# Optimization experiments

Hardware: AMD Instinct MI355X
Metric: run time of the kernel (lower is better)

The kernel has to match this reference:

```python
import jax, jax.numpy as jnp
import numpy as np

D_MODEL = 1024
NHEAD = 16
D_K = D_MODEL // NHEAD


def setup_inputs() -> dict:
    key = jax.random.key(0)
    ks = jax.random.split(key, 12)
    B, S = 1, 4096
    s = 1.0 / np.sqrt(D_MODEL)
    inp = {
        "query": jax.random.normal(ks[0], (B, S, D_MODEL), jnp.float32),
        "key": jax.random.normal(ks[1], (B, S, D_MODEL), jnp.float32),
        "value": jax.random.normal(ks[2], (B, S, D_MODEL), jnp.float32),
        "W_q": jax.random.normal(ks[3], (D_MODEL, D_MODEL), jnp.float32) * s,
        "b_q": jnp.zeros((D_MODEL,), jnp.float32),
        "W_k": jax.random.normal(ks[4], (D_MODEL, D_MODEL), jnp.float32) * s,
        "b_k": jnp.zeros((D_MODEL,), jnp.float32),
        "W_v": jax.random.normal(ks[5], (D_MODEL, D_MODEL), jnp.float32) * s,
        "b_v": jnp.zeros((D_MODEL,), jnp.float32),
        "W_o": jax.random.normal(ks[6], (D_MODEL, D_MODEL), jnp.float32) * s,
        "b_o": jnp.zeros((D_MODEL,), jnp.float32),
    }
    return inp


def reference(query, key, value, W_q, b_q, W_k, b_k, W_v, b_v, W_o, b_o):
    B, S, _ = query.shape
    # linear projections (torch Linear: x @ W.T + b)
    Q = query @ W_q.T + b_q
    K = key @ W_k.T + b_k
    V = value @ W_v.T + b_v
    # split heads: [B, S, D] -> [B, H, S, d_k]
    Q = Q.reshape(B, S, NHEAD, D_K).transpose(0, 2, 1, 3)
    K = K.reshape(B, S, NHEAD, D_K).transpose(0, 2, 1, 3)
    V = V.reshape(B, S, NHEAD, D_K).transpose(0, 2, 1, 3)
    # scaled dot-product attention (materializes [B,H,S,S] like original)
    scores = jnp.einsum("bhqd,bhkd->bhqk", Q, K) / jnp.sqrt(jnp.float32(D_K))
    weights = jax.nn.softmax(scores, axis=-1)
    attn = jnp.einsum("bhqk,bhkd->bhqd", weights, V)
    # combine heads: [B, H, S, d_k] -> [B, S, D]
    attn = attn.transpose(0, 2, 1, 3).reshape(B, S, D_MODEL)
    return attn @ W_o.T + b_o
```

## Files before the change

kernel.cpp:

```cpp
#include <hip/hip_runtime.h>
#include <hip/hip_bf16.h>
#include <type_traits>

constexpr int SEQ = 4096;
constexpr int DMODEL = 1024;
constexpr int NH = 16;
constexpr int DKH = 64;
constexpr float SCALE = 0.125f;
constexpr float SCALE2 = 0.125f * 1.4426950408889634f;

typedef __bf16 bf16x8 __attribute__((ext_vector_type(8)));
typedef __bf16 bf16x4 __attribute__((ext_vector_type(4)));
typedef float f32x4 __attribute__((ext_vector_type(4)));
typedef float f32x16 __attribute__((ext_vector_type(16)));
typedef unsigned int u32x4 __attribute__((ext_vector_type(4)));
union W8 { u32x4 u; bf16x8 v; };

__device__ inline void store_c(__hip_bfloat16* p, float v) { *p = __float2bfloat16(v); }
__device__ inline void store_c(float* p, float v) { *p = v; }

typedef const void __attribute__((address_space(1)))* gas_ptr;
typedef void __attribute__((address_space(3)))* las_ptr;
__device__ inline void load_lds_16B(const void* g, void* l) {
  __builtin_amdgcn_global_load_lds((gas_ptr)g, (las_ptr)l, 16, 0, 0);
}

__device__ inline unsigned pack2(float a, float b) {
  union { __bf16 h[2]; unsigned u; } p;
  p.h[0] = (__bf16)a; p.h[1] = (__bf16)b;
  return p.u;
}

__device__ inline void st8(__hip_bfloat16* buf, int row, int col, bf16x8 v) {
  *(bf16x8*)(buf + row * 64 + (col ^ ((row & 7) << 3))) = v;
}
__device__ inline bf16x8 ld8(const __hip_bfloat16* buf, int row, int col) {
  return *(const bf16x8*)(buf + row * 64 + (col ^ ((row & 7) << 3)));
}

__global__ __launch_bounds__(256)
void cvt_all(const float* __restrict__ q, const float* __restrict__ k,
             const float* __restrict__ v, const float* __restrict__ wq,
             const float* __restrict__ wk, const float* __restrict__ wv,
             const float* __restrict__ wo,
             __bf16* __restrict__ Xq, __bf16* __restrict__ Xk,
             __bf16* __restrict__ Xv, __bf16* __restrict__ Wqb,
             __bf16* __restrict__ Wkb, __bf16* __restrict__ Wvb,
             __bf16* __restrict__ Wob) {
  const int b = blockIdx.x;
  const float* src; __bf16* dst; size_t base;
  if      (b < 2048) { src = q;  dst = Xq;  base = b; }
  else if (b < 4096) { src = k;  dst = Xk;  base = b - 2048; }
  else if (b < 6144) { src = v;  dst = Xv;  base = b - 4096; }
  else if (b < 6656) { src = wq; dst = Wqb; base = b - 6144; }
  else if (b < 7168) { src = wk; dst = Wkb; base = b - 6656; }
  else if (b < 7680) { src = wv; dst = Wvb; base = b - 7168; }
  else               { src = wo; dst = Wob; base = b - 7680; }
  const size_t i = (base * 256 + threadIdx.x) * 8;
  const float4 a = *(const float4*)(src + i);
  const float4 c = *(const float4*)(src + i + 4);
  bf16x8 r = {(__bf16)a.x, (__bf16)a.y, (__bf16)a.z, (__bf16)a.w,
              (__bf16)c.x, (__bf16)c.y, (__bf16)c.z, (__bf16)c.w};
  *(bf16x8*)(dst + i) = r;
}

constexpr int BK = 64;

template <typename TC, bool TRANS_C>
__global__ __launch_bounds__(256)
void gemm128(const __bf16* __restrict__ A,
             const __bf16* __restrict__ W,
             const float* __restrict__ bias,
             TC* __restrict__ C,
             float out_scale) {
  __shared__ alignas(16) __bf16 As[128][64];
  __shared__ alignas(16) __bf16 Ws[64][64];

  const int t = threadIdx.x;
  const int lane = t & 63;
  const int w = t >> 6;
  const int wr = w >> 1;
  const int wc = w & 1;
  const int col = lane & 15;
  const int quad = lane >> 4;
  const int m_blk = blockIdx.y * 128;
  const int n_blk = blockIdx.x * 64;

  const int srow = t >> 3;
  const int scol = (t & 7) * 8;

  f32x4 acc[4][2] = {};

  for (int k0 = 0; k0 < DMODEL; k0 += BK) {
    __syncthreads();
    #pragma unroll
    for (int p = 0; p < 4; ++p)
      load_lds_16B(A + (size_t)(m_blk + p * 32 + srow) * DMODEL + k0 + scol,
                   &As[p * 32 + srow][scol]);
    #pragma unroll
    for (int p = 0; p < 2; ++p)
      load_lds_16B(W + (size_t)(n_blk + p * 32 + srow) * DMODEL + k0 + scol,
                   &Ws[p * 32 + srow][scol]);
    __syncthreads();

    #pragma unroll
    for (int kh = 0; kh < BK; kh += 32) {
      bf16x8 af[4], bfr[2];
      #pragma unroll
      for (int at = 0; at < 4; ++at)
        af[at] = *(const bf16x8*)&As[wr * 64 + at * 16 + col][kh + quad * 8];
      #pragma unroll
      for (int bt = 0; bt < 2; ++bt)
        bfr[bt] = *(const bf16x8*)&Ws[wc * 32 + bt * 16 + col][kh + quad * 8];
      #pragma unroll
      for (int at = 0; at < 4; ++at)
        #pragma unroll
        for (int bt = 0; bt < 2; ++bt)
          acc[at][bt] = __builtin_amdgcn_mfma_f32_16x16x32_bf16(
              af[at], bfr[bt], acc[at][bt], 0, 0, 0);
    }
  }

  #pragma unroll
  for (int at = 0; at < 4; ++at) {
    #pragma unroll
    for (int bt = 0; bt < 2; ++bt) {
      const int n = n_blk + wc * 32 + bt * 16 + col;
      const float b = bias[n];
      #pragma unroll
      for (int i = 0; i < 4; ++i) {
        const int m = m_blk + wr * 64 + at * 16 + quad * 4 + i;
        const float v = (acc[at][bt][i] + b) * out_scale;
        if constexpr (TRANS_C) store_c(&C[(size_t)n * SEQ + m], v);
        else                   store_c(&C[(size_t)m * DMODEL + n], v);
      }
    }
  }
}

__global__ __launch_bounds__(256)
void gemm_qkv(const __bf16* __restrict__ Xq, const __bf16* __restrict__ Xk,
              const __bf16* __restrict__ Xv, const __bf16* __restrict__ Wq,
              const __bf16* __restrict__ Wk, const __bf16* __restrict__ Wv,
              const float* __restrict__ bq, const float* __restrict__ bk,
              const float* __restrict__ bv,
              __hip_bfloat16* __restrict__ Cq, __hip_bfloat16* __restrict__ Ck,
              __hip_bfloat16* __restrict__ Cv) {
  __shared__ alignas(16) __bf16 As[128][64];
  __shared__ alignas(16) __bf16 Ws[64][64];

  const int z = blockIdx.z;
  const __bf16* A = (z == 0) ? Xq : (z == 1) ? Xk : Xv;
  const __bf16* W = (z == 0) ? Wq : (z == 1) ? Wk : Wv;
  const float* bias = (z == 0) ? bq : (z == 1) ? bk : bv;
  __hip_bfloat16* C = (z == 0) ? Cq : (z == 1) ? Ck : Cv;
  const float out_scale = (z == 0) ? SCALE2 : 1.0f;

  const int t = threadIdx.x;
  const int lane = t & 63;
  const int w = t >> 6;
  const int wr = w >> 1;
  const int wc = w & 1;
  const int col = lane & 15;
  const int quad = lane >> 4;
  const int m_blk = blockIdx.y * 128;
  const int n_blk = blockIdx.x * 64;

  const int srow = t >> 3;
  const int scol = (t & 7) * 8;

  f32x4 acc[4][2] = {};

  for (int k0 = 0; k0 < DMODEL; k0 += BK) {
    __syncthreads();
    #pragma unroll
    for (int p = 0; p < 4; ++p)
      load_lds_16B(A + (size_t)(m_blk + p * 32 + srow) * DMODEL + k0 + scol,
                   &As[p * 32 + srow][scol]);
    #pragma unroll
    for (int p = 0; p < 2; ++p)
      load_lds_16B(W + (size_t)(n_blk + p * 32 + srow) * DMODEL + k0 + scol,
                   &Ws[p * 32 + srow][scol]);
    __syncthreads();

    #pragma unroll
    for (int kh = 0; kh < BK; kh += 32) {
      bf16x8 af[4], bfr[2];
      #pragma unroll
      for (int at = 0; at < 4; ++at)
        af[at] = *(const bf16x8*)&As[wr * 64 + at * 16 + col][kh + quad * 8];
      #pragma unroll
      for (int bt = 0; bt < 2; ++bt)
        bfr[bt] = *(const bf16x8*)&Ws[wc * 32 + bt * 16 + col][kh + quad * 8];
      #pragma unroll
      for (int at = 0; at < 4; ++at)
        #pragma unroll
        for (int bt = 0; bt < 2; ++bt)
          acc[at][bt] = __builtin_amdgcn_mfma_f32_16x16x32_bf16(
              af[at], bfr[bt], acc[at][bt], 0, 0, 0);
    }
  }

  #pragma unroll
  for (int at = 0; at < 4; ++at) {
    #pragma unroll
    for (int bt = 0; bt < 2; ++bt) {
      const int n = n_blk + wc * 32 + bt * 16 + col;
      const float b = bias[n];
      #pragma unroll
      for (int i = 0; i < 4; ++i) {
        const int m = m_blk + wr * 64 + at * 16 + quad * 4 + i;
        const float v = (acc[at][bt][i] + b) * out_scale;
        if (z == 2) C[(size_t)n * SEQ + m] = __float2bfloat16(v);
        else        C[(size_t)m * DMODEL + n] = __float2bfloat16(v);
      }
    }
  }
}

constexpr int LDK = 72;

template <typename TA, typename TC, bool TRANS_C>
__global__ __launch_bounds__(256)
void gemm_tiled(const TA* __restrict__ A,
                const float* __restrict__ W,
                const float* __restrict__ bias,
                TC* __restrict__ C,
                float out_scale) {
  __shared__ alignas(16) __bf16 As[128][LDK];
  __shared__ alignas(16) __bf16 Ws[64][LDK];

  const int t = threadIdx.x;
  const int lane = t & 63;
  const int w = t >> 6;
  const int wr = w >> 1;
  const int wc = w & 1;
  const int col = lane & 15;
  const int quad = lane >> 4;
  const int m_blk = blockIdx.y * 128;
  const int n_blk = blockIdx.x * 64;

  f32x4 acc[4][2] = {};

  for (int k0 = 0; k0 < DMODEL; k0 += BK) {
    __syncthreads();
    if constexpr (std::is_same<TA, float>::value) {
      #pragma unroll
      for (int p = 0; p < 8; ++p) {
        const int r = p * 16 + (t >> 4);
        const int c = (t & 15) * 4;
        const float4 v =
            *(const float4*)(A + (size_t)(m_blk + r) * DMODEL + k0 + c);
        bf16x4 b = {(__bf16)v.x, (__bf16)v.y, (__bf16)v.z, (__bf16)v.w};
        *(bf16x4*)&As[r][c] = b;
      }
    } else {
      #pragma unroll
      for (int p = 0; p < 4; ++p) {
        const int r = p * 32 + (t >> 3);
        const int c = (t & 7) * 8;
        *(bf16x8*)&As[r][c] =
            *(const bf16x8*)((const __bf16*)A + (size_t)(m_blk + r) * DMODEL + k0 + c);
      }
    }
    #pragma unroll
    for (int p = 0; p < 4; ++p) {
      const int r = p * 16 + (t >> 4);
      const int c = (t & 15) * 4;
      const float4 v =
          *(const float4*)(W + (size_t)(n_blk + r) * DMODEL + k0 + c);
      bf16x4 b = {(__bf16)v.x, (__bf16)v.y, (__bf16)v.z, (__bf16)v.w};
      *(bf16x4*)&Ws[r][c] = b;
    }
    __syncthreads();

    #pragma unroll
    for (int kh = 0; kh < BK; kh += 32) {
      bf16x8 af[4], bfr[2];
      #pragma unroll
      for (int at = 0; at < 4; ++at)
        af[at] = *(const bf16x8*)&As[wr * 64 + at * 16 + col][kh + quad * 8];
      #pragma unroll
      for (int bt = 0; bt < 2; ++bt)
        bfr[bt] = *(const bf16x8*)&Ws[wc * 32 + bt * 16 + col][kh + quad * 8];
      #pragma unroll
      for (int at = 0; at < 4; ++at)
        #pragma unroll
        for (int bt = 0; bt < 2; ++bt)
          acc[at][bt] = __builtin_amdgcn_mfma_f32_16x16x32_bf16(
              af[at], bfr[bt], acc[at][bt], 0, 0, 0);
    }
  }

  #pragma unroll
  for (int at = 0; at < 4; ++at) {
    #pragma unroll
    for (int bt = 0; bt < 2; ++bt) {
      const int n = n_blk + wc * 32 + bt * 16 + col;
      const float b = bias[n];
      #pragma unroll
      for (int i = 0; i < 4; ++i) {
        const int m = m_blk + wr * 64 + at * 16 + quad * 4 + i;
        const float v = (acc[at][bt][i] + b) * out_scale;
        if constexpr (TRANS_C) store_c(&C[(size_t)n * SEQ + m], v);
        else                   store_c(&C[(size_t)m * DMODEL + n], v);
      }
    }
  }
}

__global__ __launch_bounds__(256, 4)
void flash_attn_splitN(const __hip_bfloat16* __restrict__ Q,
                       const __hip_bfloat16* __restrict__ K,
                       const __hip_bfloat16* __restrict__ Vt,
                       __hip_bfloat16* __restrict__ Op0,
                       __hip_bfloat16* __restrict__ Op1,
                       __hip_bfloat16* __restrict__ Op2,
                       __hip_bfloat16* __restrict__ Op3,
                       float* __restrict__ lsum_g) {
  __shared__ alignas(16) __hip_bfloat16 kt[64 * 64];
  __shared__ alignas(16) __hip_bfloat16 vtt[64 * 64];

  const int t = threadIdx.x;
  const int lane = t & 63;
  const int w = t >> 6;
  const int head = blockIdx.y;
  const int q0 = blockIdx.x * 128;
  const int z = blockIdx.z;
  const int nz = gridDim.z;
  const int l31 = lane & 31;
  const int hl = lane >> 5;

  __hip_bfloat16* O = (z == 0) ? Op0 : (z == 1) ? Op1 : (z == 2) ? Op2 : Op3;

  bf16x8 qf[4];
  {
    const __hip_bfloat16* qp =
        Q + (size_t)(q0 + w * 32 + l31) * DMODEL + head * DKH + hl * 8;
    #pragma unroll
    for (int db = 0; db < 4; ++db) qf[db] = *(const bf16x8*)(qp + db * 16);
  }

  f32x16 acc_o[2] = {};
  float lsa = 0.f, lsb = 0.f;

  const int sr = t >> 2;
  const int sc = (t & 3) * 16;
  const int seg = SEQ / nz;
  const int NT = seg / 64;
  const int kbeg = z * seg;

  const __hip_bfloat16* kgp = K + (size_t)(kbeg + sr) * DMODEL + head * DKH + sc;
  const __hip_bfloat16* vgp = Vt + (size_t)(head * DKH + sr) * SEQ + kbeg + sc;

  bf16x8 kr0 = *(const bf16x8*)kgp;
  bf16x8 kr1 = *(const bf16x8*)(kgp + 8);
  bf16x8 vr0 = *(const bf16x8*)vgp;
  bf16x8 vr1 = *(const bf16x8*)(vgp + 8);

  for (int ti = 0; ti < NT; ++ti) {
    __syncthreads();
    st8(kt, sr, sc, kr0);  st8(kt, sr, sc + 8, kr1);
    st8(vtt, sr, sc, vr0); st8(vtt, sr, sc + 8, vr1);
    __syncthreads();

    if (ti + 1 < NT) {
      const __hip_bfloat16* kn = kgp + (size_t)(ti + 1) * 64 * DMODEL;
      const __hip_bfloat16* vn = vgp + (ti + 1) * 64;
      kr0 = *(const bf16x8*)kn; kr1 = *(const bf16x8*)(kn + 8);
      vr0 = *(const bf16x8*)vn; vr1 = *(const bf16x8*)(vn + 8);
    }

    bf16x8 pa[4];
    #pragma unroll
    for (int kb = 0; kb < 2; ++kb) {
      f32x16 s = {};
      __builtin_amdgcn_s_setprio(1);
      #pragma unroll
      for (int db = 0; db < 4; ++db) {
        const bf16x8 kf = ld8(kt, kb * 32 + l31, db * 16 + hl * 8);
        s = __builtin_amdgcn_mfma_f32_32x32x16_bf16(kf, qf[db], s, 0, 0, 0);
      }
      __builtin_amdgcn_s_setprio(0);
      unsigned wp[8];
      #pragma unroll
      for (int i = 0; i < 8; ++i) {
        const float p0 = __builtin_amdgcn_exp2f(s[2 * i]);
        const float p1 = __builtin_amdgcn_exp2f(s[2 * i + 1]);
        lsa += p0; lsb += p1;
        wp[i] = pack2(p0, p1);
      }
      #pragma unroll
      for (int b = 0; b < 2; ++b) {
        unsigned a0 = wp[4 * b + 0], a2 = wp[4 * b + 2];
        unsigned a1 = wp[4 * b + 1], a3 = wp[4 * b + 3];
        asm("v_permlane32_swap_b32 %0, %1" : "+v"(a0), "+v"(a2));
        asm("v_permlane32_swap_b32 %0, %1" : "+v"(a1), "+v"(a3));
        W8 u;
        u.u[0] = a0; u.u[1] = a1; u.u[2] = a2; u.u[3] = a3;
        pa[kb * 2 + b] = u.v;
      }
    }

    __builtin_amdgcn_s_setprio(1);
    #pragma unroll
    for (int kq = 0; kq < 4; ++kq)
      #pragma unroll
      for (int db = 0; db < 2; ++db) {
        const bf16x8 vb = ld8(vtt, db * 32 + l31, kq * 16 + hl * 8);
        acc_o[db] = __builtin_amdgcn_mfma_f32_32x32x16_bf16(
            pa[kq], vb, acc_o[db], 0, 0, 0);
      }
    __builtin_amdgcn_s_setprio(0);
  }

  float lsumq = lsa + lsb;
  lsumq += __shfl_xor(lsumq, 32);
  if (lane < 32)
    lsum_g[((size_t)z * NH + head) * SEQ + q0 + w * 32 + lane] = lsumq;

  #pragma unroll
  for (int db = 0; db < 2; ++db) {
    #pragma unroll
    for (int r = 0; r < 16; ++r) {
      const int qr = q0 + w * 32 + (r & 3) + 8 * (r >> 2) + 4 * hl;
      const int c = head * DKH + db * 32 + l31;
      O[(size_t)qr * DMODEL + c] = __float2bfloat16(acc_o[db][r]);
    }
  }
}

__global__ __launch_bounds__(256)
void attn_combine(const __hip_bfloat16* __restrict__ Op0,
                  const __hip_bfloat16* __restrict__ Op1,
                  const __hip_bfloat16* __restrict__ Op2,
                  const __hip_bfloat16* __restrict__ Op3,
                  const float* __restrict__ ls,
                  __hip_bfloat16* __restrict__ Ao, int nz) {
  const size_t i = ((size_t)blockIdx.x * 256 + threadIdx.x) * 8;
  const int qrow = (int)(i >> 10);
  const int h = (int)((i & 1023) >> 6);
  float lsum = ls[(size_t)h * SEQ + qrow] +
               ls[(size_t)(NH + h) * SEQ + qrow];
  const bf16x8 a = *(const bf16x8*)(Op0 + i);
  const bf16x8 b = *(const bf16x8*)(Op1 + i);
  float s[8];
  #pragma unroll
  for (int j = 0; j < 8; ++j) s[j] = (float)a[j] + (float)b[j];
  if (nz == 4) {
    lsum += ls[(size_t)(2 * NH + h) * SEQ + qrow] +
            ls[(size_t)(3 * NH + h) * SEQ + qrow];
    const bf16x8 c = *(const bf16x8*)(Op2 + i);
    const bf16x8 d = *(const bf16x8*)(Op3 + i);
    #pragma unroll
    for (int j = 0; j < 8; ++j) s[j] += (float)c[j] + (float)d[j];
  }
  const float inv = 1.f / lsum;
  bf16x8 r;
  #pragma unroll
  for (int j = 0; j < 8; ++j) r[j] = (__bf16)(s[j] * inv);
  *(bf16x8*)(Ao + i) = r;
}

constexpr int LDP = 72;
constexpr float SHIFT = 8.0f;

__global__ __launch_bounds__(256)
void flash_attn_mono(const __hip_bfloat16* __restrict__ Q,
                     const __hip_bfloat16* __restrict__ K,
                     const __hip_bfloat16* __restrict__ Vt,
                     __hip_bfloat16* __restrict__ O) {
  __shared__ alignas(16) __hip_bfloat16 kt[64][LDP];
  __shared__ alignas(16) __hip_bfloat16 vtt[DKH][LDP];
  __shared__ alignas(16) __hip_bfloat16 plT[4][32][LDP];

  const int t = threadIdx.x;
  const int lane = t & 63;
  const int w = t >> 6;
  const int h = blockIdx.y;
  const int q0 = blockIdx.x * 128;
  const int col = lane & 15;
  const int quad = lane >> 4;

  bf16x8 qf[2][2];
  #pragma unroll
  for (int rg = 0; rg < 2; ++rg) {
    const __hip_bfloat16* qptr =
        Q + (size_t)(q0 + w * 32 + rg * 16 + col) * DMODEL + h * DKH + quad * 8;
    qf[rg][0] = *(const bf16x8*)qptr;
    qf[rg][1] = *(const bf16x8*)(qptr + 32);
  }

  f32x4 acc_o[2][4] = {};
  float lsumq[2] = {0.f, 0.f};
  const int sr = t >> 2;
  const int sc = (t & 3) * 16;

  for (int k0 = 0; k0 < SEQ; k0 += 64) {
    __syncthreads();
    const __hip_bfloat16* kg = K + (size_t)(k0 + sr) * DMODEL + h * DKH + sc;
    *(bf16x8*)&kt[sr][sc]     = *(const bf16x8*)kg;
    *(bf16x8*)&kt[sr][sc + 8] = *(const bf16x8*)(kg + 8);
    const __hip_bfloat16* vg = Vt + (size_t)(h * DKH + sr) * SEQ + k0 + sc;
    *(bf16x8*)&vtt[sr][sc]     = *(const bf16x8*)vg;
    *(bf16x8*)&vtt[sr][sc + 8] = *(const bf16x8*)(vg + 8);
    __syncthreads();

    #pragma unroll
    for (int jt = 0; jt < 4; ++jt) {
      const bf16x8 kf0 = *(const bf16x8*)&kt[jt * 16 + col][quad * 8];
      const bf16x8 kf1 = *(const bf16x8*)&kt[jt * 16 + col][quad * 8 + 32];
      #pragma unroll
      for (int rg = 0; rg < 2; ++rg) {
        f32x4 zz = {0.f, 0.f, 0.f, 0.f};
        zz = __builtin_amdgcn_mfma_f32_16x16x32_bf16(kf0, qf[rg][0], zz, 0, 0, 0);
        zz = __builtin_amdgcn_mfma_f32_16x16x32_bf16(kf1, qf[rg][1], zz, 0, 0, 0);
        bf16x4 pk;
        #pragma unroll
        for (int r = 0; r < 4; ++r) {
          const float p = __expf(zz[r] - SHIFT);
          lsumq[rg] += p;
          pk[r] = (__bf16)p;
        }
        *(bf16x4*)&plT[w][rg * 16 + col][jt * 16 + quad * 4] = pk;
      }
    }

    bf16x8 pa[2][2];
    #pragma unroll
    for (int rg = 0; rg < 2; ++rg) {
      pa[rg][0] = *(const bf16x8*)&plT[w][rg * 16 + col][quad * 8];
      pa[rg][1] = *(const bf16x8*)&plT[w][rg * 16 + col][quad * 8 + 32];
    }
    #pragma unroll
    for (int jt = 0; jt < 4; ++jt) {
      const bf16x8 vb0 = *(const bf16x8*)&vtt[jt * 16 + col][quad * 8];
      const bf16x8 vb1 = *(const bf16x8*)&vtt[jt * 16 + col][quad * 8 + 32];
      #pragma unroll
      for (int rg = 0; rg < 2; ++rg) {
        acc_o[rg][jt] = __builtin_amdgcn_mfma_f32_16x16x32_bf16(
            pa[rg][0], vb0, acc_o[rg][jt], 0, 0, 0);
        acc_o[rg][jt] = __builtin_amdgcn_mfma_f32_16x16x32_bf16(
            pa[rg][1], vb1, acc_o[rg][jt], 0, 0, 0);
      }
    }
  }

  #pragma unroll
  for (int rg = 0; rg < 2; ++rg) {
    lsumq[rg] += __shfl_xor(lsumq[rg], 16);
    lsumq[rg] += __shfl_xor(lsumq[rg], 32);
  }
  float invr[2][4];
  #pragma unroll
  for (int rg = 0; rg < 2; ++rg)
    #pragma unroll
    for (int r = 0; r < 4; ++r)
      invr[rg][r] = 1.f / __shfl(lsumq[rg], quad * 4 + r);

  #pragma unroll
  for (int rg = 0; rg < 2; ++rg) {
    #pragma unroll
    for (int jt = 0; jt < 4; ++jt) {
      #pragma unroll
      for (int r = 0; r < 4; ++r) {
        const int qr = q0 + w * 32 + rg * 16 + quad * 4 + r;
        const int c = h * DKH + jt * 16 + col;
        O[(size_t)qr * DMODEL + c] = __float2bfloat16(acc_o[rg][jt][r] * invr[rg][r]);
      }
    }
  }
}

extern "C" void kernel_launch(void* const* d_in, const int* in_sizes, int n_in,
                              void* d_out, int out_size, void* d_ws, size_t ws_size,
                              hipStream_t stream) {
  const float* query = (const float*)d_in[0];
  const float* key   = (const float*)d_in[1];
  const float* value = (const float*)d_in[2];
  const float* W_q   = (const float*)d_in[3];
  const float* b_q   = (const float*)d_in[4];
  const float* W_k   = (const float*)d_in[5];
  const float* b_k   = (const float*)d_in[6];
  const float* W_v   = (const float*)d_in[7];
  const float* b_v   = (const float*)d_in[8];
  const float* W_o   = (const float*)d_in[9];
  const float* b_o   = (const float*)d_in[10];

  float* out = (float*)d_out;
  const size_t mat = (size_t)SEQ * DMODEL;
  const size_t MB = 1024 * 1024;

  char* ws = (char*)d_ws;
  __hip_bfloat16* Qp = (__hip_bfloat16*)d_out;
  __hip_bfloat16* Kp = (__hip_bfloat16*)ws;
  __hip_bfloat16* Vt = Kp + mat;

  dim3 gblock(256);

  if (ws_size >= 40 * MB) {
    __bf16* Xq  = (__bf16*)((char*)d_out + 8 * MB);
    __bf16* Xk  = (__bf16*)(ws + 16 * MB);
    __bf16* Xv  = (__bf16*)(ws + 24 * MB);
    __bf16* Wqb = (__bf16*)(ws + 32 * MB);
    __bf16* Wkb = (__bf16*)(ws + 34 * MB);
    __bf16* Wvb = (__bf16*)(ws + 36 * MB);
    __bf16* Wob = (__bf16*)(ws + 38 * MB);
    __hip_bfloat16* Op0 = (__hip_bfloat16*)(ws + 16 * MB);
    __hip_bfloat16* Op1 = (__hip_bfloat16*)(ws + 24 * MB);
    __hip_bfloat16* Op2 = (__hip_bfloat16*)((char*)d_out + 8 * MB);
    __hip_bfloat16* Op3 = (__hip_bfloat16*)(ws + 40 * MB);
    float* lsum = (float*)(ws + 33 * MB);
    __hip_bfloat16* Ao = (__hip_bfloat16*)(ws + 16 * MB);

    const int nz = (ws_size >= 48 * MB) ? 4 : 2;

    hipLaunchKernelGGL(cvt_all, dim3(8192), gblock, 0, stream,
                       query, key, value, W_q, W_k, W_v, W_o,
                       Xq, Xk, Xv, Wqb, Wkb, Wvb, Wob);

    dim3 qkvgrid(DMODEL / 64, SEQ / 128, 3);
    hipLaunchKernelGGL(gemm_qkv, qkvgrid, gblock, 0, stream,
                       Xq, Xk, Xv, Wqb, Wkb, Wvb, b_q, b_k, b_v,
                       Qp, Kp, Vt);

    dim3 agrid(SEQ / 128, NH, nz);
    hipLaunchKernelGGL(flash_attn_splitN, agrid, gblock, 0, stream,
                       Qp, Kp, Vt, Op0, Op1, Op2, Op3, lsum);
    hipLaunchKernelGGL(attn_combine, dim3(2048), gblock, 0, stream,
                       Op0, Op1, Op2, Op3, lsum, Ao, nz);

    dim3 ogrid(DMODEL / 64, SEQ / 128);
    hipLaunchKernelGGL((gemm128<float, false>), ogrid, gblock, 0, stream,
                       (const __bf16*)Ao, Wob, b_o, out, 1.0f);
  } else {
    __hip_bfloat16* Ao = Qp + mat;
    float* Cw = (float*)d_ws;
    dim3 fgrid(DMODEL / 64, SEQ / 128);
    hipLaunchKernelGGL((gemm_tiled<float, __hip_bfloat16, false>), fgrid, gblock,
                       0, stream, query, W_q, b_q, Qp, SCALE);
    hipLaunchKernelGGL((gemm_tiled<float, __hip_bfloat16, false>), fgrid, gblock,
                       0, stream, key, W_k, b_k, Kp, 1.0f);
    hipLaunchKernelGGL((gemm_tiled<float, __hip_bfloat16, true>), fgrid, gblock,
                       0, stream, value, W_v, b_v, Vt, 1.0f);
    dim3 agrid(SEQ / 128, NH);
    hipLaunchKernelGGL(flash_attn_mono, agrid, gblock, 0, stream, Qp, Kp, Vt, Ao);
    hipLaunchKernelGGL((gemm_tiled<__hip_bfloat16, float, false>), fgrid, gblock,
                       0, stream, Ao, W_o, b_o, Cw, 1.0f);
    hipMemcpyAsync(out, Cw, mat * sizeof(float), hipMemcpyDeviceToDevice, stream);
  }
}
```

Baseline: 278.1 us.

## Remap block indices per XCD for L2 locality and double-buffer attention K/V tiles

Block indices in the GEMM, QKV GEMM and flash attention kernels are remapped so that blocks landing on the same XCD (assumed round-robin L&7) share contiguous M rows or head/split pairs, to improve L2 reuse of A/K/V. The attention kernel also gains double-buffered LDS for K and V tiles, so the next tile is written to the spare buffer while the current one is consumed, and one barrier per iteration replaces two. This doubles the attention LDS footprint, which may reduce occupancy under launch_bounds(256,4), and the remap relies on specific grid shapes.

```diff
diff --git a/kernel.cpp b/kernel.cpp
--- a/kernel.cpp
+++ b/kernel.cpp
@@ -83,8 +83,12 @@
   const int wc = w & 1;
   const int col = lane & 15;
   const int quad = lane >> 4;
-  const int m_blk = blockIdx.y * 128;
-  const int n_blk = blockIdx.x * 64;
+
+  const int L = blockIdx.x + 16 * blockIdx.y;
+  const int xcd = L & 7;
+  const int c = L >> 3;
+  const int m_blk = (xcd * 4 + (c >> 4)) * 128;
+  const int n_blk = (c & 15) * 64;
 
   const int srow = t >> 3;
   const int scol = (t & 7) * 8;
@@ -149,12 +153,91 @@
   __shared__ alignas(16) __bf16 As[128][64];
   __shared__ alignas(16) __bf16 Ws[64][64];
 
-  const int z = blockIdx.z;
+  const int L = blockIdx.x + 16 * (blockIdx.y + 32 * blockIdx.z);
+  const int xcd = L & 7;
+  const int cc = L >> 3;
+  const int z = cc / 64;
+  const int c2 = cc & 63;
+  const int m_blk = (xcd * 4 + (c2 >> 4)) * 128;
+  const int n_blk = (c2 & 15) * 64;
+
   const __bf16* A = (z == 0) ? Xq : (z == 1) ? Xk : Xv;
   const __bf16* W = (z == 0) ? Wq : (z == 1) ? Wk : Wv;
   const float* bias = (z == 0) ? bq : (z == 1) ? bk : bv;
   __hip_bfloat16* C = (z == 0) ? Cq : (z == 1) ? Ck : Cv;
   const float out_scale = (z == 0) ? SCALE2 : 1.0f;
+
+  const int t = threadIdx.x;
+  const int lane = t & 63;
+  const int w = t >> 6;
+  const int wr = w >> 1;
+  const int wc = w & 1;
+  const int col = lane & 15;
+  const int quad = lane >> 4;
+
+  const int srow = t >> 3;
+  const int scol = (t & 7) * 8;
+
+  f32x4 acc[4][2] = {};
+
+  for (int k0 = 0; k0 < DMODEL; k0 += BK) {
+    __syncthreads();
+    #pragma unroll
+    for (int p = 0; p < 4; ++p)
+      load_lds_16B(A + (size_t)(m_blk + p * 32 + srow) * DMODEL + k0 + scol,
+                   &As[p * 32 + srow][scol]);
+    #pragma unroll
+    for (int p = 0; p < 2; ++p)
+      load_lds_16B(W + (size_t)(n_blk + p * 32 + srow) * DMODEL + k0 + scol,
+                   &Ws[p * 32 + srow][scol]);
+    __syncthreads();
+
+    #pragma unroll
+    for (int kh = 0; kh < BK; kh += 32) {
+      bf16x8 af[4], bfr[2];
+      #pragma unroll
+      for (int at = 0; at < 4; ++at)
+        af[at] = *(const bf16x8*)&As[wr * 64 + at * 16 + col][kh + quad * 8];
+      #pragma unroll
+      for (int bt = 0; bt < 2; ++bt)
+        bfr[bt] = *(const bf16x8*)&Ws[wc * 32 + bt * 16 + col][kh + quad * 8];
+      #pragma unroll
+      for (int at = 0; at < 4; ++at)
+        #pragma unroll
+        for (int bt = 0; bt < 2; ++bt)
+          acc[at][bt] = __builtin_amdgcn_mfma_f32_16x16x32_bf16(
+              af[at], bfr[bt], acc[at][bt], 0, 0, 0);
+    }
+  }
+
+  #pragma unroll
+  for (int at = 0; at < 4; ++at) {
+    #pragma unroll
+    for (int bt = 0; bt < 2; ++bt) {
+      const int n = n_blk + wc * 32 + bt * 16 + col;
+      const float b = bias[n];
+      #pragma unroll
+      for (int i = 0; i < 4; ++i) {
+        const int m = m_blk + wr * 64 + at * 16 + quad * 4 + i;
+        const float v = (acc[at][bt][i] + b) * out_scale;
+        if (z == 2) C[(size_t)n * SEQ + m] = __float2bfloat16(v);
+        else        C[(size_t)m * DMODEL + n] = __float2bfloat16(v);
+      }
+    }
+  }
+}
+
+constexpr int LDK = 72;
+
+template <typename TA, typename TC, bool TRANS_C>
+__global__ __launch_bounds__(256)
+void gemm_tiled(const TA* __restrict__ A,
+                const float* __restrict__ W,
+                const float* __restrict__ bias,
+                TC* __restrict__ C,
+                float out_scale) {
+  __shared__ alignas(16) __bf16 As[128][LDK];
+  __shared__ alignas(16) __bf16 Ws[64][LDK];
 
   const int t = threadIdx.x;
   const int lane = t & 63;
@@ -166,80 +249,6 @@
   const int m_blk = blockIdx.y * 128;
   const int n_blk = blockIdx.x * 64;
 
-  const int srow = t >> 3;
-  const int scol = (t & 7) * 8;
-
-  f32x4 acc[4][2] = {};
-
-  for (int k0 = 0; k0 < DMODEL; k0 += BK) {
-    __syncthreads();
-    #pragma unroll
-    for (int p = 0; p < 4; ++p)
-      load_lds_16B(A + (size_t)(m_blk + p * 32 + srow) * DMODEL + k0 + scol,
-                   &As[p * 32 + srow][scol]);
-    #pragma unroll
-    for (int p = 0; p < 2; ++p)
-      load_lds_16B(W + (size_t)(n_blk + p * 32 + srow) * DMODEL + k0 + scol,
-                   &Ws[p * 32 + srow][scol]);
-    __syncthreads();
-
-    #pragma unroll
-    for (int kh = 0; kh < BK; kh += 32) {
-      bf16x8 af[4], bfr[2];
-      #pragma unroll
-      for (int at = 0; at < 4; ++at)
-        af[at] = *(const bf16x8*)&As[wr * 64 + at * 16 + col][kh + quad * 8];
-      #pragma unroll
-      for (int bt = 0; bt < 2; ++bt)
-        bfr[bt] = *(const bf16x8*)&Ws[wc * 32 + bt * 16 + col][kh + quad * 8];
-      #pragma unroll
-      for (int at = 0; at < 4; ++at)
-        #pragma unroll
-        for (int bt = 0; bt < 2; ++bt)
-          acc[at][bt] = __builtin_amdgcn_mfma_f32_16x16x32_bf16(
-              af[at], bfr[bt], acc[at][bt], 0, 0, 0);
-    }
-  }
-
-  #pragma unroll
-  for (int at = 0; at < 4; ++at) {
-    #pragma unroll
-    for (int bt = 0; bt < 2; ++bt) {
-      const int n = n_blk + wc * 32 + bt * 16 + col;
-      const float b = bias[n];
-      #pragma unroll
-      for (int i = 0; i < 4; ++i) {
-        const int m = m_blk + wr * 64 + at * 16 + quad * 4 + i;
-        const float v = (acc[at][bt][i] + b) * out_scale;
-        if (z == 2) C[(size_t)n * SEQ + m] = __float2bfloat16(v);
-        else        C[(size_t)m * DMODEL + n] = __float2bfloat16(v);
-      }
-    }
-  }
-}
-
-constexpr int LDK = 72;
-
-template <typename TA, typename TC, bool TRANS_C>
-__global__ __launch_bounds__(256)
-void gemm_tiled(const TA* __restrict__ A,
-                const float* __restrict__ W,
-                const float* __restrict__ bias,
-                TC* __restrict__ C,
-                float out_scale) {
-  __shared__ alignas(16) __bf16 As[128][LDK];
-  __shared__ alignas(16) __bf16 Ws[64][LDK];
-
-  const int t = threadIdx.x;
-  const int lane = t & 63;
-  const int w = t >> 6;
-  const int wr = w >> 1;
-  const int wc = w & 1;
-  const int col = lane & 15;
-  const int quad = lane >> 4;
-  const int m_blk = blockIdx.y * 128;
-  const int n_blk = blockIdx.x * 64;
-
   f32x4 acc[4][2] = {};
 
   for (int k0 = 0; k0 < DMODEL; k0 += BK) {
@@ -318,18 +327,23 @@
                        __hip_bfloat16* __restrict__ Op2,
                        __hip_bfloat16* __restrict__ Op3,
                        float* __restrict__ lsum_g) {
-  __shared__ alignas(16) __hip_bfloat16 kt[64 * 64];
-  __shared__ alignas(16) __hip_bfloat16 vtt[64 * 64];
+  __shared__ alignas(16) __hip_bfloat16 kt[2][64 * 64];
+  __shared__ alignas(16) __hip_bfloat16 vtt[2][64 * 64];
 
   const int t = threadIdx.x;
   const int lane = t & 63;
   const int w = t >> 6;
-  const int head = blockIdx.y;
-  const int q0 = blockIdx.x * 128;
-  const int z = blockIdx.z;
   const int nz = gridDim.z;
   const int l31 = lane & 31;
   const int hl = lane >> 5;
+
+  const int L = blockIdx.x + 32 * (blockIdx.y + 16 * blockIdx.z);
+  const int xcd = L & 7;
+  const int c = L >> 3;
+  const int pair = xcd * (2 * nz) + (c >> 5);
+  const int q0 = (c & 31) * 128;
+  const int head = pair & 15;
+  const int z = pair >> 4;
 
   __hip_bfloat16* O = (z == 0) ? Op0 : (z == 1) ? Op1 : (z == 2) ? Op2 : Op3;
 
@@ -357,18 +371,30 @@
   bf16x8 kr1 = *(const bf16x8*)(kgp + 8);
   bf16x8 vr0 = *(const bf16x8*)vgp;
   bf16x8 vr1 = *(const bf16x8*)(vgp + 8);
+  st8(kt[0], sr, sc, kr0);  st8(kt[0], sr, sc + 8, kr1);
+  st8(vtt[0], sr, sc, vr0); st8(vtt[0], sr, sc + 8, vr1);
+  if (NT > 1) {
+    kr0 = *(const bf16x8*)(kgp + (size_t)64 * DMODEL);
+    kr1 = *(const bf16x8*)(kgp + (size_t)64 * DMODEL + 8);
+    vr0 = *(const bf16x8*)(vgp + 64);
+    vr1 = *(const bf16x8*)(vgp + 64 + 8);
+  }
+  __syncthreads();
 
   for (int ti = 0; ti < NT; ++ti) {
-    __syncthreads();
-    st8(kt, sr, sc, kr0);  st8(kt, sr, sc + 8, kr1);
-    st8(vtt, sr, sc, vr0); st8(vtt, sr, sc + 8, vr1);
-    __syncthreads();
+    const int cur = ti & 1;
+    const __hip_bfloat16* ktc = kt[cur];
+    const __hip_bfloat16* vtc = vtt[cur];
 
     if (ti + 1 < NT) {
-      const __hip_bfloat16* kn = kgp + (size_t)(ti + 1) * 64 * DMODEL;
-      const __hip_bfloat16* vn = vgp + (ti + 1) * 64;
-      kr0 = *(const bf16x8*)kn; kr1 = *(const bf16x8*)(kn + 8);
-      vr0 = *(const bf16x8*)vn; vr1 = *(const bf16x8*)(vn + 8);
+      st8(kt[cur ^ 1], sr, sc, kr0);  st8(kt[cur ^ 1], sr, sc + 8, kr1);
+      st8(vtt[cur ^ 1], sr, sc, vr0); st8(vtt[cur ^ 1], sr, sc + 8, vr1);
+      if (ti + 2 < NT) {
+        const __hip_bfloat16* kn = kgp + (size_t)(ti + 2) * 64 * DMODEL;
+        const __hip_bfloat16* vn = vgp + (ti + 2) * 64;
+        kr0 = *(const bf16x8*)kn; kr1 = *(const bf16x8*)(kn + 8);
+        vr0 = *(const bf16x8*)vn; vr1 = *(const bf16x8*)(vn + 8);
+      }
     }
 
     bf16x8 pa[4];
@@ -378,7 +404,7 @@
       __builtin_amdgcn_s_setprio(1);
       #pragma unroll
       for (int db = 0; db < 4; ++db) {
-        const bf16x8 kf = ld8(kt, kb * 32 + l31, db * 16 + hl * 8);
+        const bf16x8 kf = ld8(ktc, kb * 32 + l31, db * 16 + hl * 8);
         s = __builtin_amdgcn_mfma_f32_32x32x16_bf16(kf, qf[db], s, 0, 0, 0);
       }
       __builtin_amdgcn_s_setprio(0);
@@ -407,11 +433,13 @@
     for (int kq = 0; kq < 4; ++kq)
       #pragma unroll
       for (int db = 0; db < 2; ++db) {
-        const bf16x8 vb = ld8(vtt, db * 32 + l31, kq * 16 + hl * 8);
+        const bf16x8 vb = ld8(vtc, db * 32 + l31, kq * 16 + hl * 8);
         acc_o[db] = __builtin_amdgcn_mfma_f32_32x32x16_bf16(
             pa[kq], vb, acc_o[db], 0, 0, 0);
       }
     __builtin_amdgcn_s_setprio(0);
+
+    __syncthreads();
   }
 
   float lsumq = lsa + lsb;
@@ -424,8 +452,8 @@
     #pragma unroll
     for (int r = 0; r < 16; ++r) {
       const int qr = q0 + w * 32 + (r & 3) + 8 * (r >> 2) + 4 * hl;
-      const int c = head * DKH + db * 32 + l31;
-      O[(size_t)qr * DMODEL + c] = __float2bfloat16(acc_o[db][r]);
+      const int cidx = head * DKH + db * 32 + l31;
+      O[(size_t)qr * DMODEL + cidx] = __float2bfloat16(acc_o[db][r]);
     }
   }
 }
```

After: 281.4 us. Within noise of the previous version (+1.2%).

## Remap GEMM blocks per XCD and split attention launch into two head halves

Applied to the files above, without the earlier changes.

The gemm128 and gemm_qkv kernels now remap the linear block index so that each of the 8 XCDs (chosen by round-robin dispatch) gets a contiguous band of M rows. This is meant to improve L2 reuse of the A tiles within each XCD's private cache. The flash attention launch is split into two launches of eight heads each, passed through a new head0 parameter, which may change cache locality or scheduling. The cost is one extra kernel launch, and the remap relies on the hardware dispatching blocks round-robin across XCDs.

```diff
diff --git a/kernel.cpp b/kernel.cpp
--- a/kernel.cpp
+++ b/kernel.cpp
@@ -83,8 +83,12 @@
   const int wc = w & 1;
   const int col = lane & 15;
   const int quad = lane >> 4;
-  const int m_blk = blockIdx.y * 128;
-  const int n_blk = blockIdx.x * 64;
+
+  const int L = blockIdx.x + 16 * blockIdx.y;
+  const int xcd = L & 7;
+  const int c = L >> 3;
+  const int m_blk = (xcd * 4 + (c >> 4)) * 128;
+  const int n_blk = (c & 15) * 64;
 
   const int srow = t >> 3;
   const int scol = (t & 7) * 8;
@@ -149,12 +153,91 @@
   __shared__ alignas(16) __bf16 As[128][64];
   __shared__ alignas(16) __bf16 Ws[64][64];
 
-  const int z = blockIdx.z;
+  const int L = blockIdx.x + 16 * (blockIdx.y + 32 * blockIdx.z);
+  const int xcd = L & 7;
+  const int cc = L >> 3;
+  const int z = cc / 64;
+  const int c2 = cc & 63;
+  const int m_blk = (xcd * 4 + (c2 >> 4)) * 128;
+  const int n_blk = (c2 & 15) * 64;
+
   const __bf16* A = (z == 0) ? Xq : (z == 1) ? Xk : Xv;
   const __bf16* W = (z == 0) ? Wq : (z == 1) ? Wk : Wv;
   const float* bias = (z == 0) ? bq : (z == 1) ? bk : bv;
   __hip_bfloat16* C = (z == 0) ? Cq : (z == 1) ? Ck : Cv;
   const float out_scale = (z == 0) ? SCALE2 : 1.0f;
+
+  const int t = threadIdx.x;
+  const int lane = t & 63;
+  const int w = t >> 6;
+  const int wr = w >> 1;
+  const int wc = w & 1;
+  const int col = lane & 15;
+  const int quad = lane >> 4;
+
+  const int srow = t >> 3;
+  const int scol = (t & 7) * 8;
+
+  f32x4 acc[4][2] = {};
+
+  for (int k0 = 0; k0 < DMODEL; k0 += BK) {
+    __syncthreads();
+    #pragma unroll
+    for (int p = 0; p < 4; ++p)
+      load_lds_16B(A + (size_t)(m_blk + p * 32 + srow) * DMODEL + k0 + scol,
+                   &As[p * 32 + srow][scol]);
+    #pragma unroll
+    for (int p = 0; p < 2; ++p)
+      load_lds_16B(W + (size_t)(n_blk + p * 32 + srow) * DMODEL + k0 + scol,
+                   &Ws[p * 32 + srow][scol]);
+    __syncthreads();
+
+    #pragma unroll
+    for (int kh = 0; kh < BK; kh += 32) {
+      bf16x8 af[4], bfr[2];
+      #pragma unroll
+      for (int at = 0; at < 4; ++at)
+        af[at] = *(const bf16x8*)&As[wr * 64 + at * 16 + col][kh + quad * 8];
+      #pragma unroll
+      for (int bt = 0; bt < 2; ++bt)
+        bfr[bt] = *(const bf16x8*)&Ws[wc * 32 + bt * 16 + col][kh + quad * 8];
+      #pragma unroll
+      for (int at = 0; at < 4; ++at)
+        #pragma unroll
+        for (int bt = 0; bt < 2; ++bt)
+          acc[at][bt] = __builtin_amdgcn_mfma_f32_16x16x32_bf16(
+              af[at], bfr[bt], acc[at][bt], 0, 0, 0);
+    }
+  }
+
+  #pragma unroll
+  for (int at = 0; at < 4; ++at) {
+    #pragma unroll
+    for (int bt = 0; bt < 2; ++bt) {
+      const int n = n_blk + wc * 32 + bt * 16 + col;
+      const float b = bias[n];
+      #pragma unroll
+      for (int i = 0; i < 4; ++i) {
+        const int m = m_blk + wr * 64 + at * 16 + quad * 4 + i;
+        const float v = (acc[at][bt][i] + b) * out_scale;
+        if (z == 2) C[(size_t)n * SEQ + m] = __float2bfloat16(v);
+        else        C[(size_t)m * DMODEL + n] = __float2bfloat16(v);
+      }
+    }
+  }
+}
+
+constexpr int LDK = 72;
+
+template <typename TA, typename TC, bool TRANS_C>
+__global__ __launch_bounds__(256)
+void gemm_tiled(const TA* __restrict__ A,
+                const float* __restrict__ W,
+                const float* __restrict__ bias,
+                TC* __restrict__ C,
+                float out_scale) {
+  __shared__ alignas(16) __bf16 As[128][LDK];
+  __shared__ alignas(16) __bf16 Ws[64][LDK];
 
   const int t = threadIdx.x;
   const int lane = t & 63;
@@ -166,80 +249,6 @@
   const int m_blk = blockIdx.y * 128;
   const int n_blk = blockIdx.x * 64;
 
-  const int srow = t >> 3;
-  const int scol = (t & 7) * 8;
-
-  f32x4 acc[4][2] = {};
-
-  for (int k0 = 0; k0 < DMODEL; k0 += BK) {
-    __syncthreads();
-    #pragma unroll
-    for (int p = 0; p < 4; ++p)
-      load_lds_16B(A + (size_t)(m_blk + p * 32 + srow) * DMODEL + k0 + scol,
-                   &As[p * 32 + srow][scol]);
-    #pragma unroll
-    for (int p = 0; p < 2; ++p)
-      load_lds_16B(W + (size_t)(n_blk + p * 32 + srow) * DMODEL + k0 + scol,
-                   &Ws[p * 32 + srow][scol]);
-    __syncthreads();
-
-    #pragma unroll
-    for (int kh = 0; kh < BK; kh += 32) {
-      bf16x8 af[4], bfr[2];
-      #pragma unroll
-      for (int at = 0; at < 4; ++at)
-        af[at] = *(const bf16x8*)&As[wr * 64 + at * 16 + col][kh + quad * 8];
-      #pragma unroll
-      for (int bt = 0; bt < 2; ++bt)
-        bfr[bt] = *(const bf16x8*)&Ws[wc * 32 + bt * 16 + col][kh + quad * 8];
-      #pragma unroll
-      for (int at = 0; at < 4; ++at)
-        #pragma unroll
-        for (int bt = 0; bt < 2; ++bt)
-          acc[at][bt] = __builtin_amdgcn_mfma_f32_16x16x32_bf16(
-              af[at], bfr[bt], acc[at][bt], 0, 0, 0);
-    }
-  }
-
-  #pragma unroll
-  for (int at = 0; at < 4; ++at) {
-    #pragma unroll
-    for (int bt = 0; bt < 2; ++bt) {
-      const int n = n_blk + wc * 32 + bt * 16 + col;
-      const float b = bias[n];
-      #pragma unroll
-      for (int i = 0; i < 4; ++i) {
-        const int m = m_blk + wr * 64 + at * 16 + quad * 4 + i;
-        const float v = (acc[at][bt][i] + b) * out_scale;
-        if (z == 2) C[(size_t)n * SEQ + m] = __float2bfloat16(v);
-        else        C[(size_t)m * DMODEL + n] = __float2bfloat16(v);
-      }
-    }
-  }
-}
-
-constexpr int LDK = 72;
-
-template <typename TA, typename TC, bool TRANS_C>
-__global__ __launch_bounds__(256)
-void gemm_tiled(const TA* __restrict__ A,
-                const float* __restrict__ W,
-                const float* __restrict__ bias,
-                TC* __restrict__ C,
-                float out_scale) {
-  __shared__ alignas(16) __bf16 As[128][LDK];
-  __shared__ alignas(16) __bf16 Ws[64][LDK];
-
-  const int t = threadIdx.x;
-  const int lane = t & 63;
-  const int w = t >> 6;
-  const int wr = w >> 1;
-  const int wc = w & 1;
-  const int col = lane & 15;
-  const int quad = lane >> 4;
-  const int m_blk = blockIdx.y * 128;
-  const int n_blk = blockIdx.x * 64;
-
   f32x4 acc[4][2] = {};
 
   for (int k0 = 0; k0 < DMODEL; k0 += BK) {
@@ -317,14 +326,14 @@
                        __hip_bfloat16* __restrict__ Op1,
                        __hip_bfloat16* __restrict__ Op2,
                        __hip_bfloat16* __restrict__ Op3,
-                       float* __restrict__ lsum_g) {
+                       float* __restrict__ lsum_g, int head0) {
   __shared__ alignas(16) __hip_bfloat16 kt[64 * 64];
   __shared__ alignas(16) __hip_bfloat16 vtt[64 * 64];
 
   const int t = threadIdx.x;
   const int lane = t & 63;
   const int w = t >> 6;
-  const int head = blockIdx.y;
+  const int head = head0 + blockIdx.y;
   const int q0 = blockIdx.x * 128;
   const int z = blockIdx.z;
   const int nz = gridDim.z;
@@ -424,8 +433,8 @@
     #pragma unroll
     for (int r = 0; r < 16; ++r) {
       const int qr = q0 + w * 32 + (r & 3) + 8 * (r >> 2) + 4 * hl;
-      const int c = head * DKH + db * 32 + l31;
-      O[(size_t)qr * DMODEL + c] = __float2bfloat16(acc_o[db][r]);
+      const int cidx = head * DKH + db * 32 + l31;
+      O[(size_t)qr * DMODEL + cidx] = __float2bfloat16(acc_o[db][r]);
     }
   }
 }
@@ -624,9 +633,11 @@
                        Xq, Xk, Xv, Wqb, Wkb, Wvb, b_q, b_k, b_v,
                        Qp, Kp, Vt);
 
-    dim3 agrid(SEQ / 128, NH, nz);
+    dim3 agrid(SEQ / 128, NH / 2, nz);
     hipLaunchKernelGGL(flash_attn_splitN, agrid, gblock, 0, stream,
-                       Qp, Kp, Vt, Op0, Op1, Op2, Op3, lsum);
+                       Qp, Kp, Vt, Op0, Op1, Op2, Op3, lsum, 0);
+    hipLaunchKernelGGL(flash_attn_splitN, agrid, gblock, 0, stream,
+                       Qp, Kp, Vt, Op0, Op1, Op2, Op3, lsum, NH / 2);
     hipLaunchKernelGGL(attn_combine, dim3(2048), gblock, 0, stream,
                        Op0, Op1, Op2, Op3, lsum, Ao, nz);
 
```

Measured after the change: 285.8 us. +2.8%, slower.

## Rewrite QKV projection as 256x256 double-buffered 8-wave GEMM, swizzle output GEMM blocks

Applied to the files above, without the earlier changes.

Replaces the 128x64 QKV projection GEMM with a 256x256 tile kernel using 512 threads, double-buffered LDS staging via direct global-to-LDS loads, and phased MFMA compute interleaved with prefetch under explicit waitcnt and barriers. The larger tiles raise arithmetic intensity and the pipelining hides global load latency behind MFMA work. Separately, the output GEMM remaps block indices so blocks on the same XCD share rows of A, aiming at better L2 reuse. The new kernel uses 128KB of LDS and many accumulator registers, which limits occupancy, and the hand-written vmcnt counts must match the outstanding load order exactly.

```diff
diff --git a/kernel.cpp b/kernel.cpp
--- a/kernel.cpp
+++ b/kernel.cpp
@@ -83,8 +83,12 @@
   const int wc = w & 1;
   const int col = lane & 15;
   const int quad = lane >> 4;
-  const int m_blk = blockIdx.y * 128;
-  const int n_blk = blockIdx.x * 64;
+
+  const int L = blockIdx.x + 16 * blockIdx.y;
+  const int xcd = L & 7;
+  const int c = L >> 3;
+  const int m_blk = (xcd * 4 + (c >> 4)) * 128;
+  const int n_blk = (c & 15) * 64;
 
   const int srow = t >> 3;
   const int scol = (t & 7) * 8;
@@ -138,84 +142,135 @@
   }
 }
 
-__global__ __launch_bounds__(256)
-void gemm_qkv(const __bf16* __restrict__ Xq, const __bf16* __restrict__ Xk,
-              const __bf16* __restrict__ Xv, const __bf16* __restrict__ Wq,
-              const __bf16* __restrict__ Wk, const __bf16* __restrict__ Wv,
-              const float* __restrict__ bq, const float* __restrict__ bk,
-              const float* __restrict__ bv,
-              __hip_bfloat16* __restrict__ Cq, __hip_bfloat16* __restrict__ Ck,
-              __hip_bfloat16* __restrict__ Cv) {
-  __shared__ alignas(16) __bf16 As[128][64];
-  __shared__ alignas(16) __bf16 Ws[64][64];
+__device__ __forceinline__ void stage_half_256(const __bf16* src, __bf16* dst,
+                                               int t) {
+  const int sr = t >> 3;
+  const int sc2 = (t & 7) * 8;
+  #pragma unroll
+  for (int r = 0; r < 2; ++r)
+    load_lds_16B(src + (size_t)(r * 64 + sr) * DMODEL + sc2,
+                 dst + (r * 64 + sr) * 64 + sc2);
+}
+
+template <int MH, int NHF>
+__device__ __forceinline__ void qkv_phase(const __bf16* Asb, const __bf16* Wsb,
+                                          int wm, int wn, int col, int quad,
+                                          f32x4 (&acc)[8][4],
+                                          const __bf16* stage_src,
+                                          __bf16* stage_dst, int t,
+                                          bool do_vmcnt) {
+  bf16x8 af[4][2], bfr[2][2];
+  #pragma unroll
+  for (int fm = 0; fm < 4; ++fm)
+    #pragma unroll
+    for (int kh = 0; kh < 2; ++kh)
+      af[fm][kh] = *(const bf16x8*)&Asb[(MH * 128 + wm * 64 + fm * 16 + col) * 64 +
+                                        kh * 32 + quad * 8];
+  #pragma unroll
+  for (int fn = 0; fn < 2; ++fn)
+    #pragma unroll
+    for (int kh = 0; kh < 2; ++kh)
+      bfr[fn][kh] = *(const bf16x8*)&Wsb[(NHF * 128 + wn * 32 + fn * 16 + col) * 64 +
+                                         kh * 32 + quad * 8];
+  stage_half_256(stage_src, stage_dst, t);
+  __builtin_amdgcn_s_barrier();
+  asm volatile("s_waitcnt lgkmcnt(0)" ::: "memory");
+  __builtin_amdgcn_sched_barrier(0);
+  __builtin_amdgcn_s_setprio(1);
+  #pragma unroll
+  for (int kh = 0; kh < 2; ++kh)
+    #pragma unroll
+    for (int fm = 0; fm < 4; ++fm)
+      #pragma unroll
+      for (int fn = 0; fn < 2; ++fn)
+        acc[MH * 4 + fm][NHF * 2 + fn] = __builtin_amdgcn_mfma_f32_16x16x32_bf16(
+            af[fm][kh], bfr[fn][kh], acc[MH * 4 + fm][NHF * 2 + fn], 0, 0, 0);
+  __builtin_amdgcn_s_setprio(0);
+  if (do_vmcnt) asm volatile("s_waitcnt vmcnt(4)" ::: "memory");
+  __builtin_amdgcn_s_barrier();
+}
+
+__global__ __launch_bounds__(512, 2)
+void gemm_qkv8(const __bf16* __restrict__ Xq, const __bf16* __restrict__ Xk,
+               const __bf16* __restrict__ Xv, const __bf16* __restrict__ Wq,
+               const __bf16* __restrict__ Wk, const __bf16* __restrict__ Wv,
+               const float* __restrict__ bq, const float* __restrict__ bk,
+               const float* __restrict__ bv,
+               __hip_bfloat16* __restrict__ Cq, __hip_bfloat16* __restrict__ Ck,
+               __hip_bfloat16* __restrict__ Cv) {
+  __shared__ alignas(16) __bf16 lds_all[4][256 * 64];
+  __bf16* As0 = &lds_all[0][0];
+  __bf16* As1 = &lds_all[1][0];
+  __bf16* Ws0 = &lds_all[2][0];
+  __bf16* Ws1 = &lds_all[3][0];
 
   const int z = blockIdx.z;
   const __bf16* A = (z == 0) ? Xq : (z == 1) ? Xk : Xv;
   const __bf16* W = (z == 0) ? Wq : (z == 1) ? Wk : Wv;
   const float* bias = (z == 0) ? bq : (z == 1) ? bk : bv;
   __hip_bfloat16* C = (z == 0) ? Cq : (z == 1) ? Ck : Cv;
-  const float out_scale = (z == 0) ? SCALE2 : 1.0f;
+  const float osc = (z == 0) ? SCALE2 : 1.0f;
 
   const int t = threadIdx.x;
   const int lane = t & 63;
-  const int w = t >> 6;
-  const int wr = w >> 1;
-  const int wc = w & 1;
+  const int wave = t >> 6;
+  const int wm = wave >> 2;
+  const int wn = wave & 3;
   const int col = lane & 15;
   const int quad = lane >> 4;
-  const int m_blk = blockIdx.y * 128;
-  const int n_blk = blockIdx.x * 64;
-
-  const int srow = t >> 3;
-  const int scol = (t & 7) * 8;
-
-  f32x4 acc[4][2] = {};
-
-  for (int k0 = 0; k0 < DMODEL; k0 += BK) {
-    __syncthreads();
-    #pragma unroll
-    for (int p = 0; p < 4; ++p)
-      load_lds_16B(A + (size_t)(m_blk + p * 32 + srow) * DMODEL + k0 + scol,
-                   &As[p * 32 + srow][scol]);
-    #pragma unroll
-    for (int p = 0; p < 2; ++p)
-      load_lds_16B(W + (size_t)(n_blk + p * 32 + srow) * DMODEL + k0 + scol,
-                   &Ws[p * 32 + srow][scol]);
-    __syncthreads();
-
-    #pragma unroll
-    for (int kh = 0; kh < BK; kh += 32) {
-      bf16x8 af[4], bfr[2];
-      #pragma unroll
-      for (int at = 0; at < 4; ++at)
-        af[at] = *(const bf16x8*)&As[wr * 64 + at * 16 + col][kh + quad * 8];
-      #pragma unroll
-      for (int bt = 0; bt < 2; ++bt)
-        bfr[bt] = *(const bf16x8*)&Ws[wc * 32 + bt * 16 + col][kh + quad * 8];
-      #pragma unroll
-      for (int at = 0; at < 4; ++at)
-        #pragma unroll
-        for (int bt = 0; bt < 2; ++bt)
-          acc[at][bt] = __builtin_amdgcn_mfma_f32_16x16x32_bf16(
-              af[at], bfr[bt], acc[at][bt], 0, 0, 0);
-    }
-  }
-
-  #pragma unroll
-  for (int at = 0; at < 4; ++at) {
-    #pragma unroll
-    for (int bt = 0; bt < 2; ++bt) {
-      const int n = n_blk + wc * 32 + bt * 16 + col;
-      const float b = bias[n];
+  const int n_blk = blockIdx.x * 256;
+  const int m_blk = blockIdx.y * 256;
+
+  constexpr int NKT = DMODEL / 64;
+  constexpr int NIT = NKT / 2;
+
+  auto srcA = [&](int kt, int h) {
+    return A + (size_t)(m_blk + h * 128) * DMODEL + kt * 64;
+  };
+  auto srcB = [&](int kt, int h) {
+    return W + (size_t)(n_blk + h * 128) * DMODEL + kt * 64;
+  };
+
+  f32x4 acc[8][4] = {};
+
+  stage_half_256(srcA(0, 0), As0, t);
+  stage_half_256(srcA(0, 1), As0 + 128 * 64, t);
+  stage_half_256(srcB(0, 0), Ws0, t);
+  stage_half_256(srcB(0, 1), Ws0 + 128 * 64, t);
+  stage_half_256(srcA(1, 0), As1, t);
+  stage_half_256(srcB(1, 0), Ws1, t);
+  asm volatile("s_waitcnt vmcnt(4)" ::: "memory");
+  __builtin_amdgcn_s_barrier();
+
+  for (int it = 0; it < NIT; ++it) {
+    const int j = 2 * it;
+    const int kt1 = j + 1;
+    const int kt2 = (j + 2 < NKT) ? j + 2 : NKT - 1;
+    const int kt3 = (j + 3 < NKT) ? j + 3 : NKT - 1;
+    qkv_phase<0, 0>(As0, Ws0, wm, wn, col, quad, acc, srcA(kt1, 1), As1 + 128 * 64, t, false);
+    qkv_phase<0, 1>(As0, Ws0, wm, wn, col, quad, acc, srcB(kt1, 1), Ws1 + 128 * 64, t, false);
+    qkv_phase<1, 0>(As0, Ws0, wm, wn, col, quad, acc, srcA(kt2, 0), As0, t, false);
+    qkv_phase<1, 1>(As0, Ws0, wm, wn, col, quad, acc, srcB(kt2, 0), Ws0, t, true);
+    qkv_phase<0, 0>(As1, Ws1, wm, wn, col, quad, acc, srcA(kt2, 1), As0 + 128 * 64, t, false);
+    qkv_phase<0, 1>(As1, Ws1, wm, wn, col, quad, acc, srcB(kt2, 1), Ws0 + 128 * 64, t, false);
+    qkv_phase<1, 0>(As1, Ws1, wm, wn, col, quad, acc, srcA(kt3, 0), As1, t, false);
+    qkv_phase<1, 1>(As1, Ws1, wm, wn, col, quad, acc, srcB(kt3, 0), Ws1, t, true);
+  }
+
+  #pragma unroll
+  for (int fm = 0; fm < 8; ++fm)
+    #pragma unroll
+    for (int fn = 0; fn < 4; ++fn) {
+      const int n = n_blk + (fn >> 1) * 128 + wn * 32 + (fn & 1) * 16 + col;
+      const float bb = bias[n];
       #pragma unroll
       for (int i = 0; i < 4; ++i) {
-        const int m = m_blk + wr * 64 + at * 16 + quad * 4 + i;
-        const float v = (acc[at][bt][i] + b) * out_scale;
+        const int m = m_blk + (fm >> 2) * 128 + wm * 64 + (fm & 3) * 16 + quad * 4 + i;
+        const float v = (acc[fm][fn][i] + bb) * osc;
         if (z == 2) C[(size_t)n * SEQ + m] = __float2bfloat16(v);
         else        C[(size_t)m * DMODEL + n] = __float2bfloat16(v);
       }
     }
-  }
 }
 
 constexpr int LDK = 72;
@@ -424,8 +479,8 @@
     #pragma unroll
     for (int r = 0; r < 16; ++r) {
       const int qr = q0 + w * 32 + (r & 3) + 8 * (r >> 2) + 4 * hl;
-      const int c = head * DKH + db * 32 + l31;
-      O[(size_t)qr * DMODEL + c] = __float2bfloat16(acc_o[db][r]);
+      const int cidx = head * DKH + db * 32 + l31;
+      O[(size_t)qr * DMODEL + cidx] = __float2bfloat16(acc_o[db][r]);
     }
   }
 }
@@ -619,8 +674,8 @@
                        query, key, value, W_q, W_k, W_v, W_o,
                        Xq, Xk, Xv, Wqb, Wkb, Wvb, Wob);
 
-    dim3 qkvgrid(DMODEL / 64, SEQ / 128, 3);
-    hipLaunchKernelGGL(gemm_qkv, qkvgrid, gblock, 0, stream,
+    dim3 qkvgrid(DMODEL / 256, SEQ / 256, 3);
+    hipLaunchKernelGGL(gemm_qkv8, qkvgrid, dim3(512), 0, stream,
                        Xq, Xk, Xv, Wqb, Wkb, Wvb, b_q, b_k, b_v,
                        Qp, Kp, Vt);
 
```

Result: slower. 320.1 us (+15.1%).
